# Performance work log

Measured on AMD Instinct MI355X. Metric: run time of the kernel, lower is better.

The kernel has to match this reference:

```python
import jax, jax.numpy as jnp
import numpy as np
from jax import lax

# Fixed-point scales (powers of two, as in linger's luna/venus pipeline).
# scale_gi = input_scale * weight_ih_scale, scale_gh = hidden_scale * weight_hh_scale.
SCALE_GI = 2.0 ** 14
SCALE_GH = 2.0 ** 14
Q27 = 2.0 ** 27
Q15 = 2.0 ** 15
Q31 = 2.0 ** 31
INT32_MIN = -(2.0 ** 31)
INT32_MAX = 2.0 ** 31 - 1


def quant_round(x, scale):
    # QuantMode.floor_add: floor(x*scale + 0.5)/scale, with straight-through gradient
    # (linger QAT rounding uses STE).
    q = jnp.floor(x * scale + 0.5) / scale
    return x + lax.stop_gradient(q - x)


@jax.custom_vjp
def qsigmoid(x):
    # Quantize input to Q27 int32, evaluate sigmoid, output Q31 -> requant to Q15.
    i_q27 = jnp.clip(jnp.floor(x * Q27 + 0.5), INT32_MIN, INT32_MAX)
    s = jax.nn.sigmoid(i_q27 / Q27)
    out_q31 = jnp.floor(s * Q31 + 0.5)
    out_q15 = jnp.floor(out_q31 * (2.0 ** -16) + 0.5)  # luna_requant(31 -> 15)
    return out_q15 / Q15

def _qsig_fwd(x):
    return qsigmoid(x), x

def _qsig_bwd(x, g):
    s = jax.nn.sigmoid(x)
    return (g * s * (1.0 - s),)

qsigmoid.defvjp(_qsig_fwd, _qsig_bwd)


@jax.custom_vjp
def qtanh(x):
    i_q27 = jnp.clip(jnp.floor(x * Q27 + 0.5), INT32_MIN, INT32_MAX)
    t = jnp.tanh(i_q27 / Q27)
    out_q31 = jnp.floor(t * Q31 + 0.5)
    out_q15 = jnp.floor(out_q31 * (2.0 ** -16) + 0.5)
    return out_q15 / Q15

def _qtanh_fwd(x):
    return qtanh(x), x

def _qtanh_bwd(x, g):
    t = jnp.tanh(x)
    return (g * (1.0 - t * t),)

qtanh.defvjp(_qtanh_fwd, _qtanh_bwd)


def setup_inputs() -> dict:
    key = jax.random.key(0)
    k = jax.random.split(key, 6)
    B, I, H = 8192, 512, 512
    return {
        "input_x": jax.random.normal(k[0], (B, I), dtype=jnp.float32),
        "hidden": jax.random.normal(k[1], (B, H), dtype=jnp.float32),
        "weight_ih": jax.random.normal(k[2], (3 * H, I), dtype=jnp.float32) * 0.05,
        "weight_hh": jax.random.normal(k[3], (3 * H, H), dtype=jnp.float32) * 0.05,
        "bias_ih": jax.random.normal(k[4], (3 * H,), dtype=jnp.float32) * 0.05,
        "bias_hh": jax.random.normal(k[5], (3 * H,), dtype=jnp.float32) * 0.05,
    }


def reference(input_x, hidden, weight_ih, weight_hh, bias_ih, bias_hh):
    # Dense gate projections: [B, 3H]
    gi = input_x @ weight_ih.T + bias_ih
    gh = hidden @ weight_hh.T + bias_hh
    # Requant gate pre-activations to fixed-point grid (biasih/biashh quantizers)
    gi = quant_round(gi, SCALE_GI)
    gh = quant_round(gh, SCALE_GH)
    i_r, i_i, i_n = jnp.split(gi, 3, axis=1)
    h_r, h_i, h_n = jnp.split(gh, 3, axis=1)
    resetgate = qsigmoid(i_r + h_r)
    inputgate = qsigmoid(i_i + h_i)
    # h_n requantized to Q27, reset*h_n product requantized to Q15
    h_n = quant_round(h_n, Q27)
    resetgate_h_n = quant_round(resetgate * h_n, Q15)
    newgate = qtanh(resetgate_h_n + i_n)
    new_hidden = quant_round(hidden, Q15)
    hy = newgate + inputgate * (new_hidden - newgate)
    return hy
```

## Files before the change

### kernel.cpp

```cpp
#include <hip/hip_runtime.h>
#include <math.h>


typedef _Float16 f16x8  __attribute__((ext_vector_type(8)));
typedef _Float16 f16x4  __attribute__((ext_vector_type(4)));
typedef __bf16   bf16x8 __attribute__((ext_vector_type(8)));
typedef float    f32x16 __attribute__((ext_vector_type(16)));

namespace {

constexpr int Bsz = 8192, Ksz = 512, Hsz = 512;
constexpr int BM = 64, BN = 64;

constexpr unsigned WCH0    = 16384u;
constexpr unsigned NCHUNK  = 16384u + 3072u;
constexpr unsigned WS_F16  = NCHUNK * 512u;
constexpr size_t   WS_NEED = (size_t)WS_F16 * 2;

__device__ __forceinline__ float qround(float x, float s, float invs) {
    return floorf(x * s + 0.5f) * invs;
}

__device__ __forceinline__ float qsigmoid_dev(float x) {
    float iq = floorf(x * 134217728.0f + 0.5f);
    iq = fminf(fmaxf(iq, -2147483648.0f), 2147483648.0f);
    float e = __expf(-iq * 7.450580596923828125e-9f);
    float s = __builtin_amdgcn_rcpf(1.0f + e);
    float q31 = floorf(s * 2147483648.0f + 0.5f);
    float q15 = floorf(q31 * 1.52587890625e-5f + 0.5f);
    return q15 * 3.0517578125e-5f;
}

__device__ __forceinline__ float qtanh_dev(float x) {
    float iq = floorf(x * 134217728.0f + 0.5f);
    iq = fminf(fmaxf(iq, -2147483648.0f), 2147483648.0f);
    float z = iq * 7.450580596923828125e-9f;
    float e = __expf(2.0f * z);
    float t = 1.0f - 2.0f * __builtin_amdgcn_rcpf(e + 1.0f);
    float q31 = floorf(t * 2147483648.0f + 0.5f);
    float q15 = floorf(q31 * 1.52587890625e-5f + 0.5f);
    return q15 * 3.0517578125e-5f;
}

__device__ __forceinline__ void dma16(const void* g, void* l) {
    __builtin_amdgcn_global_load_lds(
        (const __attribute__((address_space(1))) unsigned int*)g,
        (__attribute__((address_space(3))) unsigned int*)l, 16, 0, 0);
}

__device__ __forceinline__ void split2(float a, float b, unsigned& hi, unsigned& lo) {
    unsigned ua = __float_as_uint(a); ua += 0x7fffu + ((ua >> 16) & 1u);
    unsigned ub = __float_as_uint(b); ub += 0x7fffu + ((ub >> 16) & 1u);
    hi = (ua >> 16) | (ub & 0xffff0000u);
    float ra = a - __uint_as_float(ua & 0xffff0000u);
    float rb = b - __uint_as_float(ub & 0xffff0000u);
    unsigned va = __float_as_uint(ra); va += 0x7fffu + ((va >> 16) & 1u);
    unsigned vb = __float_as_uint(rb); vb += 0x7fffu + ((vb >> 16) & 1u);
    lo = (va >> 16) | (vb & 0xffff0000u);
}

}

__global__ __launch_bounds__(256) void cvt_lds_f16(
    const float* __restrict__ x, const float* __restrict__ h,
    const float* __restrict__ wih, const float* __restrict__ whh,
    _Float16* __restrict__ ws)
{
    __shared__ __align__(16) _Float16 lt[8192];

    const int b2  = blockIdx.x;
    const int b   = b2 >> 1;
    const int kha = b2 & 1;
    const int tid = threadIdx.x;

    const float* src;
    unsigned chbase;
    if (b < 512) {
        const int arr = b >> 8, M32 = b & 255;
        src = (arr ? h : x) + (size_t)M32 * 32u * 512u;
        chbase = (unsigned)arr * 8192u + (unsigned)M32 * 32u;
    } else {
        const int w = b - 512;
        const int g = w >> 4, N32 = w & 15;
        const int rowLocal = (g % 3) * 512 + N32 * 32;
        src = (g < 3 ? wih : whh) + (size_t)rowLocal * 512u;
        chbase = WCH0 + (unsigned)((g * 16 + N32) * 32);
    }
    src += kha * 256;

#pragma unroll
    for (int rep = 0; rep < 8; ++rep) {
        const int idx = rep * 256 + tid;
        const int row = idx >> 6;
        const int q   = idx & 63;
        const float4 v = *(const float4*)(src + (size_t)row * 512 + q * 4);
        const int K16l = q >> 2;
        const int kh   = (q >> 1) & 1;
        const int half = (q & 1) * 4;
        const int rsw  = (row + (q >> 1)) & 31;
        f16x4 o;
        o[0] = (_Float16)v.x; o[1] = (_Float16)v.y;
        o[2] = (_Float16)v.z; o[3] = (_Float16)v.w;
        *(f16x4*)&lt[K16l * 512 + kh * 256 + rsw * 8 + half] = o;
    }
    __syncthreads();

    const int wid = tid >> 6, lane = tid & 63;
    const int kh  = lane >> 5, row = lane & 31;
#pragma unroll
    for (int cc = 0; cc < 4; ++cc) {
        const int K16l = wid * 4 + cc;
        const int rsw  = (row + 2 * K16l + kh) & 31;
        const f16x8 o = *(const f16x8*)&lt[K16l * 512 + kh * 256 + rsw * 8];
        *(f16x8*)(ws + (size_t)(chbase + (unsigned)(kha * 16 + K16l)) * 512u
                      + lane * 8) = o;
    }
}

__global__ __launch_bounds__(256, 4) void qgru_f16_occ(
    const _Float16* __restrict__ ws, const float* __restrict__ hid,
    const float* __restrict__ bih, const float* __restrict__ bhh,
    float* __restrict__ out)
{
    __shared__ __align__(16) _Float16 lds[16384];

    const int t = threadIdx.x, lane = t & 63, wid = t >> 6;
    const int mt = wid >> 1, nt = wid & 1;
    const int m0 = blockIdx.x * BM, n0 = blockIdx.y * BN;

    unsigned goff[4];
    int      ldst[4];
#pragma unroll
    for (int c = 0; c < 4; ++c) {
        const int idx = wid * 4 + c;
        unsigned ch; int lo;
        if (idx < 4) {
            const int arr = idx >> 1, mtc = idx & 1;
            ch = (unsigned)arr * 8192u + (unsigned)((m0 >> 5) + mtc) * 32u;
            lo = idx * 512;
        } else {
            const int w = idx - 4, g = w >> 1, ntc = w & 1;
            ch = WCH0 + (unsigned)((g * 16 + (n0 >> 5) + ntc) * 32);
            lo = 2048 + w * 512;
        }
        goff[c] = ch * 1024u + (unsigned)lane * 16u;
        ldst[c] = lo;
    }

    f32x16 acc[6];
#pragma unroll
    for (int g = 0; g < 6; ++g)
#pragma unroll
        for (int i = 0; i < 16; ++i) acc[g][i] = 0.0f;

    const char* wsb = (const char*)ws;
    const int lr = lane & 31, lk8 = (lane >> 5) * 8;

#pragma unroll
    for (int c = 0; c < 4; ++c)
        dma16(wsb + goff[c], &lds[ldst[c]]);

    for (int step = 0; step < 32; ++step) {
        __syncthreads();

        if (step + 1 < 32) {
            const unsigned kb = (unsigned)(step + 1) * 1024u;
            const int nb = ((step + 1) & 1) * 8192;
#pragma unroll
            for (int c = 0; c < 4; ++c)
                dma16(wsb + goff[c] + kb, &lds[nb + ldst[c]]);
        }

        const int cb = (step & 1) * 8192;
        const int lfo = cb + lk8 * 32 + lr * 8;
        const f16x8 ax = *(const f16x8*)&lds[lfo + (0 + mt) * 512];
        const f16x8 ah = *(const f16x8*)&lds[lfo + (2 + mt) * 512];
#pragma unroll
        for (int g = 0; g < 6; ++g) {
            const f16x8 b = *(const f16x8*)&lds[lfo + 2048 + (g * 2 + nt) * 512];
            acc[g] = __builtin_amdgcn_mfma_f32_32x32x16_f16(
                         g < 3 ? ax : ah, b, acc[g], 0, 0, 0);
        }
    }

    constexpr float S14 = 16384.0f,     I14 = 1.0f / 16384.0f;
    constexpr float S15 = 32768.0f,     I15 = 1.0f / 32768.0f;
    constexpr float S27 = 134217728.0f, I27 = 1.0f / 134217728.0f;

    const int lh = lane >> 5, l32 = lane & 31;
    const int n = n0 + nt * 32 + l32;
    const float br = bih[n], bi = bih[n + 512], bn = bih[n + 1024];
    const float cr = bhh[n], ci = bhh[n + 512], cn = bhh[n + 1024];

#pragma unroll
    for (int r = 0; r < 16; ++r) {
        const int row = (r & 3) + 8 * (r >> 2) + 4 * lh;
        const int m   = m0 + mt * 32 + row;
        const float hv = hid[(size_t)m * Hsz + n];

        float gir = qround(acc[0][r] + br, S14, I14);
        float gii = qround(acc[1][r] + bi, S14, I14);
        float gin = qround(acc[2][r] + bn, S14, I14);
        float ghr = qround(acc[3][r] + cr, S14, I14);
        float ghi = qround(acc[4][r] + ci, S14, I14);
        float ghn = qround(acc[5][r] + cn, S14, I14);
        float resetg = qsigmoid_dev(gir + ghr);
        float inputg = qsigmoid_dev(gii + ghi);
        float hn  = qround(ghn, S27, I27);
        float rh  = qround(resetg * hn, S15, I15);
        float newg = qtanh_dev(rh + gin);
        float nh  = qround(hv, S15, I15);
        out[(size_t)m * Hsz + n] = newg + inputg * (nh - newg);
    }
}

__global__ __launch_bounds__(256, 2) void qgru_mfma_bf16x3(
    const float* __restrict__ x, const float* __restrict__ hid,
    const float* __restrict__ wih, const float* __restrict__ whh,
    const float* __restrict__ bih, const float* __restrict__ bhh,
    float* __restrict__ out)
{
    __shared__ __align__(16) unsigned short lds[16384];

    const int t = threadIdx.x, lane = t & 63, wid = t >> 6;
    const int mt = wid >> 1, nt = wid & 1;
    const int m0 = blockIdx.x * BM, n0 = blockIdx.y * BN;
    const int s_r = t >> 2, s_k = (t & 3) << 2;
    const int s_kh = s_k >> 3, s_j = s_k & 7, s_rt = s_r >> 5, s_r32 = s_r & 31;

    const float* gA[2];
    gA[0] = x   + (size_t)(m0 + s_r) * Ksz + s_k;
    gA[1] = hid + (size_t)(m0 + s_r) * Ksz + s_k;
    const float* gW[6];
#pragma unroll
    for (int g = 0; g < 3; ++g) {
        gW[g]     = wih + (size_t)(g * Hsz + n0 + s_r) * Ksz + s_k;
        gW[g + 3] = whh + (size_t)(g * Hsz + n0 + s_r) * Ksz + s_k;
    }
    const int lh = lane >> 5, l32 = lane & 31;

    f32x16 acc[6];
#pragma unroll
    for (int g = 0; g < 6; ++g)
#pragma unroll
        for (int i = 0; i < 16; ++i) acc[g][i] = 0.0f;

    float4 vA[2], vW[6];
#pragma unroll
    for (int tt = 0; tt < 2; ++tt) vA[tt] = *(const float4*)gA[tt];
#pragma unroll
    for (int g = 0; g < 6; ++g)    vW[g]  = *(const float4*)gW[g];

    for (int k0 = 0; k0 < Ksz; k0 += 16) {
        __syncthreads();
#pragma unroll
        for (int tt = 0; tt < 2; ++tt) {
            unsigned h0, h1, l0, l1;
            split2(vA[tt].x, vA[tt].y, h0, l0);
            split2(vA[tt].z, vA[tt].w, h1, l1);
            unsigned bH = ((((tt*2+0)*2+s_rt)*2+s_kh)*32+s_r32)*8 + s_j;
            unsigned bL = ((((tt*2+1)*2+s_rt)*2+s_kh)*32+s_r32)*8 + s_j;
            *reinterpret_cast<uint2*>(&lds[bH]) = make_uint2(h0, h1);
            *reinterpret_cast<uint2*>(&lds[bL]) = make_uint2(l0, l1);
        }
#pragma unroll
        for (int g = 0; g < 6; ++g) {
            unsigned h0, h1, l0, l1;
            split2(vW[g].x, vW[g].y, h0, l0);
            split2(vW[g].z, vW[g].w, h1, l1);
            unsigned bH = 4096u + ((((g*2+0)*2+s_rt)*2+s_kh)*32+s_r32)*8 + s_j;
            unsigned bL = 4096u + ((((g*2+1)*2+s_rt)*2+s_kh)*32+s_r32)*8 + s_j;
            *reinterpret_cast<uint2*>(&lds[bH]) = make_uint2(h0, h1);
            *reinterpret_cast<uint2*>(&lds[bL]) = make_uint2(l0, l1);
        }
        __syncthreads();
        const int kn = (k0 + 16 < Ksz) ? (k0 + 16) : 0;
#pragma unroll
        for (int tt = 0; tt < 2; ++tt) vA[tt] = *(const float4*)(gA[tt] + kn);
#pragma unroll
        for (int g = 0; g < 6; ++g)    vW[g]  = *(const float4*)(gW[g] + kn);

        const bf16x8 ax_hi = *reinterpret_cast<const bf16x8*>(&lds[((((0)*2+mt)*2+lh)*32+l32)*8]);
        const bf16x8 ax_lo = *reinterpret_cast<const bf16x8*>(&lds[((((1)*2+mt)*2+lh)*32+l32)*8]);
        const bf16x8 ah_hi = *reinterpret_cast<const bf16x8*>(&lds[((((2)*2+mt)*2+lh)*32+l32)*8]);
        const bf16x8 ah_lo = *reinterpret_cast<const bf16x8*>(&lds[((((3)*2+mt)*2+lh)*32+l32)*8]);
#pragma unroll
        for (int g = 0; g < 6; ++g) {
            const bf16x8 b_hi = *reinterpret_cast<const bf16x8*>(&lds[4096u + ((((g*2+0)*2+nt)*2+lh)*32+l32)*8]);
            const bf16x8 b_lo = *reinterpret_cast<const bf16x8*>(&lds[4096u + ((((g*2+1)*2+nt)*2+lh)*32+l32)*8]);
            const bf16x8 a_hi = (g < 3) ? ax_hi : ah_hi;
            const bf16x8 a_lo = (g < 3) ? ax_lo : ah_lo;
            acc[g] = __builtin_amdgcn_mfma_f32_32x32x16_bf16(a_hi, b_hi, acc[g], 0, 0, 0);
            acc[g] = __builtin_amdgcn_mfma_f32_32x32x16_bf16(a_hi, b_lo, acc[g], 0, 0, 0);
            acc[g] = __builtin_amdgcn_mfma_f32_32x32x16_bf16(a_lo, b_hi, acc[g], 0, 0, 0);
        }
    }

    constexpr float S14 = 16384.0f,     I14 = 1.0f / 16384.0f;
    constexpr float S15 = 32768.0f,     I15 = 1.0f / 32768.0f;
    constexpr float S27 = 134217728.0f, I27 = 1.0f / 134217728.0f;
    const int n = n0 + nt * 32 + l32;
    const float br = bih[n], bi = bih[n + 512], bn = bih[n + 1024];
    const float cr = bhh[n], ci = bhh[n + 512], cn = bhh[n + 1024];
#pragma unroll
    for (int r = 0; r < 16; ++r) {
        const int row = (r & 3) + 8 * (r >> 2) + 4 * lh;
        const int m   = m0 + mt * 32 + row;
        const float hv = hid[(size_t)m * Hsz + n];
        float gir = qround(acc[0][r] + br, S14, I14);
        float gii = qround(acc[1][r] + bi, S14, I14);
        float gin = qround(acc[2][r] + bn, S14, I14);
        float ghr = qround(acc[3][r] + cr, S14, I14);
        float ghi = qround(acc[4][r] + ci, S14, I14);
        float ghn = qround(acc[5][r] + cn, S14, I14);
        float resetg = qsigmoid_dev(gir + ghr);
        float inputg = qsigmoid_dev(gii + ghi);
        float hn  = qround(ghn, S27, I27);
        float rh  = qround(resetg * hn, S15, I15);
        float newg = qtanh_dev(rh + gin);
        float nh  = qround(hv, S15, I15);
        out[(size_t)m * Hsz + n] = newg + inputg * (nh - newg);
    }
}

extern "C" void kernel_launch(void* const* d_in, const int* in_sizes, int n_in,
                              void* d_out, int out_size, void* d_ws, size_t ws_size,
                              hipStream_t stream) {
    const float* x   = (const float*)d_in[0];
    const float* hid = (const float*)d_in[1];
    const float* wih = (const float*)d_in[2];
    const float* whh = (const float*)d_in[3];
    const float* bih = (const float*)d_in[4];
    const float* bhh = (const float*)d_in[5];
    float* out = (float*)d_out;
    dim3 grid(Bsz / BM, Hsz / BN);

    if (ws_size >= WS_NEED) {
        cvt_lds_f16<<<1216, 256, 0, stream>>>(
            x, hid, wih, whh, (_Float16*)d_ws);
        qgru_f16_occ<<<grid, dim3(256), 0, stream>>>(
            (const _Float16*)d_ws, hid, bih, bhh, out);
    } else {
        qgru_mfma_bf16x3<<<grid, dim3(256), 0, stream>>>(
            x, hid, wih, whh, bih, bhh, out);
    }
}
```

Baseline: 129.9 us.

## Fuse activation f16 conversion into GEMM kernel, pre-convert only weights

```diff
diff --git a/kernel.cpp b/kernel.cpp
--- a/kernel.cpp
+++ b/kernel.cpp
@@ -61,32 +61,22 @@
 
 }
 
-__global__ __launch_bounds__(256) void cvt_lds_f16(
-    const float* __restrict__ x, const float* __restrict__ h,
+__global__ __launch_bounds__(256) void cvt_w_f16(
     const float* __restrict__ wih, const float* __restrict__ whh,
     _Float16* __restrict__ ws)
 {
     __shared__ __align__(16) _Float16 lt[8192];
 
     const int b2  = blockIdx.x;
-    const int b   = b2 >> 1;
+    const int w   = b2 >> 1;
     const int kha = b2 & 1;
     const int tid = threadIdx.x;
 
-    const float* src;
-    unsigned chbase;
-    if (b < 512) {
-        const int arr = b >> 8, M32 = b & 255;
-        src = (arr ? h : x) + (size_t)M32 * 32u * 512u;
-        chbase = (unsigned)arr * 8192u + (unsigned)M32 * 32u;
-    } else {
-        const int w = b - 512;
-        const int g = w >> 4, N32 = w & 15;
-        const int rowLocal = (g % 3) * 512 + N32 * 32;
-        src = (g < 3 ? wih : whh) + (size_t)rowLocal * 512u;
-        chbase = WCH0 + (unsigned)((g * 16 + N32) * 32);
-    }
-    src += kha * 256;
+    const int g = w >> 4, N32 = w & 15;
+    const int rowLocal = (g % 3) * 512 + N32 * 32;
+    const float* src = (g < 3 ? wih : whh)
+                     + (size_t)rowLocal * 512u + (size_t)kha * 256u;
+    const unsigned chbase = WCH0 + (unsigned)((g * 16 + N32) * 32);
 
 #pragma unroll
     for (int rep = 0; rep < 8; ++rep) {
@@ -105,11 +95,11 @@
     }
     __syncthreads();
 
-    const int wid = tid >> 6, lane = tid & 63;
-    const int kh  = lane >> 5, row = lane & 31;
+    const int wv = tid >> 6, lane = tid & 63;
+    const int kh = lane >> 5, row = lane & 31;
 #pragma unroll
     for (int cc = 0; cc < 4; ++cc) {
-        const int K16l = wid * 4 + cc;
+        const int K16l = wv * 4 + cc;
         const int rsw  = (row + 2 * K16l + kh) & 31;
         const f16x8 o = *(const f16x8*)&lt[K16l * 512 + kh * 256 + rsw * 8];
         *(f16x8*)(ws + (size_t)(chbase + (unsigned)(kha * 16 + K16l)) * 512u
@@ -117,8 +107,9 @@
     }
 }
 
-__global__ __launch_bounds__(256, 4) void qgru_f16_occ(
-    const _Float16* __restrict__ ws, const float* __restrict__ hid,
+__global__ __launch_bounds__(256, 4) void qgru_f16_fuseA(
+    const float* __restrict__ x, const float* __restrict__ hid,
+    const _Float16* __restrict__ ws,
     const float* __restrict__ bih, const float* __restrict__ bhh,
     float* __restrict__ out)
 {
@@ -128,24 +119,24 @@
     const int mt = wid >> 1, nt = wid & 1;
     const int m0 = blockIdx.x * BM, n0 = blockIdx.y * BN;
 
-    unsigned goff[4];
-    int      ldst[4];
-#pragma unroll
-    for (int c = 0; c < 4; ++c) {
-        const int idx = wid * 4 + c;
-        unsigned ch; int lo;
-        if (idx < 4) {
-            const int arr = idx >> 1, mtc = idx & 1;
-            ch = (unsigned)arr * 8192u + (unsigned)((m0 >> 5) + mtc) * 32u;
-            lo = idx * 512;
-        } else {
-            const int w = idx - 4, g = w >> 1, ntc = w & 1;
-            ch = WCH0 + (unsigned)((g * 16 + (n0 >> 5) + ntc) * 32);
-            lo = 2048 + w * 512;
-        }
-        goff[c] = ch * 1024u + (unsigned)lane * 16u;
-        ldst[c] = lo;
-    }
+    unsigned goffW[3];
+    int      ldstW[3];
+#pragma unroll
+    for (int c = 0; c < 3; ++c) {
+        const int wp = wid * 3 + c;
+        const int g = wp >> 1, ntc = wp & 1;
+        const unsigned ch = WCH0 + (unsigned)((g * 16 + (n0 >> 5) + ntc) * 32);
+        goffW[c] = ch * 1024u + (unsigned)lane * 16u;
+        ldstW[c] = 2048 + wp * 512;
+    }
+
+    const int arr = wid >> 1, mtc = wid & 1;
+    const float* srcA = (arr ? hid : x) + (size_t)(m0 + mtc * 32) * 512u;
+    const int r32a = lane >> 2, sega = lane & 3;
+    const size_t ga0 = (size_t)r32a * 512u + (size_t)(sega * 4);
+    const size_t ga1 = ga0 + 16u * 512u;
+    const int aoff0 = wid * 512 + (sega >> 1) * 256 + r32a * 8 + (sega & 1) * 4;
+    const int aoff1 = aoff0 + 128;
 
     f32x16 acc[6];
 #pragma unroll
@@ -156,9 +147,22 @@
     const char* wsb = (const char*)ws;
     const int lr = lane & 31, lk8 = (lane >> 5) * 8;
 
-#pragma unroll
-    for (int c = 0; c < 4; ++c)
-        dma16(wsb + goff[c], &lds[ldst[c]]);
+    float4 vA0 = *(const float4*)(srcA + ga0);
+    float4 vA1 = *(const float4*)(srcA + ga1);
+#pragma unroll
+    for (int c = 0; c < 3; ++c)
+        dma16(wsb + goffW[c], &lds[ldstW[c]]);
+    {
+        f16x4 o0, o1;
+        o0[0] = (_Float16)vA0.x; o0[1] = (_Float16)vA0.y;
+        o0[2] = (_Float16)vA0.z; o0[3] = (_Float16)vA0.w;
+        o1[0] = (_Float16)vA1.x; o1[1] = (_Float16)vA1.y;
+        o1[2] = (_Float16)vA1.z; o1[3] = (_Float16)vA1.w;
+        *(f16x4*)&lds[aoff0] = o0;
+        *(f16x4*)&lds[aoff1] = o1;
+    }
+    vA0 = *(const float4*)(srcA + 16 + ga0);
+    vA1 = *(const float4*)(srcA + 16 + ga1);
 
     for (int step = 0; step < 32; ++step) {
         __syncthreads();
@@ -167,8 +171,20 @@
             const unsigned kb = (unsigned)(step + 1) * 1024u;
             const int nb = ((step + 1) & 1) * 8192;
 #pragma unroll
-            for (int c = 0; c < 4; ++c)
-                dma16(wsb + goff[c] + kb, &lds[nb + ldst[c]]);
+            for (int c = 0; c < 3; ++c)
+                dma16(wsb + goffW[c] + kb, &lds[nb + ldstW[c]]);
+            f16x4 o0, o1;
+            o0[0] = (_Float16)vA0.x; o0[1] = (_Float16)vA0.y;
+            o0[2] = (_Float16)vA0.z; o0[3] = (_Float16)vA0.w;
+            o1[0] = (_Float16)vA1.x; o1[1] = (_Float16)vA1.y;
+            o1[2] = (_Float16)vA1.z; o1[3] = (_Float16)vA1.w;
+            *(f16x4*)&lds[nb + aoff0] = o0;
+            *(f16x4*)&lds[nb + aoff1] = o1;
+            if (step + 2 < 32) {
+                const size_t ko = (size_t)(step + 2) * 16u;
+                vA0 = *(const float4*)(srcA + ko + ga0);
+                vA1 = *(const float4*)(srcA + ko + ga1);
+            }
         }
 
         const int cb = (step & 1) * 8192;
@@ -336,10 +352,9 @@
     dim3 grid(Bsz / BM, Hsz / BN);
 
     if (ws_size >= WS_NEED) {
-        cvt_lds_f16<<<1216, 256, 0, stream>>>(
-            x, hid, wih, whh, (_Float16*)d_ws);
-        qgru_f16_occ<<<grid, dim3(256), 0, stream>>>(
-            (const _Float16*)d_ws, hid, bih, bhh, out);
+        cvt_w_f16<<<192, 256, 0, stream>>>(wih, whh, (_Float16*)d_ws);
+        qgru_f16_fuseA<<<grid, dim3(256), 0, stream>>>(
+            x, hid, (const _Float16*)d_ws, bih, bhh, out);
     } else {
         qgru_mfma_bf16x3<<<grid, dim3(256), 0, stream>>>(
             x, hid, wih, whh, bih, bhh, out);
```

New measurement: 133.4 us. 2.8% more time.
